# Performance work log

Measured on AMD Instinct MI355X. Metric: run time of the kernel, lower is better.

## Reference

```python
import jax, jax.numpy as jnp
import numpy as np

L = 4; B = 128; S = 128; N = B * S; E = 262144
IN = 64; HID = 128; PE = 16; HEADS = 4; DK = HID // HEADS; OUT = 10


def setup_inputs() -> dict:
    key = jax.random.key(0)
    ks = iter(jax.random.split(key, 64))
    def nrm(shape, scale=1.0):
        return jax.random.normal(next(ks), shape, jnp.float32) * scale
    inp = {
        'x': nrm((N, IN)),
        'pe': nrm((N, PE)),
        'edge_attr': nrm((E, HID)),
        'sph': jax.random.uniform(next(ks), (B, 1, S, S), jnp.float32),
        'node_w': nrm((IN, HID - PE), 0.05), 'node_b': jnp.zeros((HID - PE,), jnp.float32),
        'pe_w': nrm((PE, PE), 0.05), 'pe_b': jnp.zeros((PE,), jnp.float32),
        'conv_Aw': nrm((L, HID, HID), 0.05), 'conv_Ab': jnp.zeros((L, HID), jnp.float32),
        'conv_Bw': nrm((L, HID, HID), 0.05), 'conv_Bb': jnp.zeros((L, HID), jnp.float32),
        'conv_Cw': nrm((L, HID, HID), 0.05), 'conv_Cb': jnp.zeros((L, HID), jnp.float32),
        'conv_Dw': nrm((L, HID, HID), 0.05), 'conv_Db': jnp.zeros((L, HID), jnp.float32),
        'conv_Ew': nrm((L, HID, HID), 0.05), 'conv_Eb': jnp.zeros((L, HID), jnp.float32),
        'bnx_g': jnp.ones((L, HID), jnp.float32), 'bnx_b': jnp.zeros((L, HID), jnp.float32),
        'bne_g': jnp.ones((L, HID), jnp.float32), 'bne_b': jnp.zeros((L, HID), jnp.float32),
        'attn_w': nrm((4, HID, HID), 0.05), 'attn_b': jnp.zeros((4, HID), jnp.float32),
        'mlp1_w': nrm((HID, HID // 2), 0.05), 'mlp1_b': jnp.zeros((HID // 2,), jnp.float32),
        'mlp2_w': nrm((HID // 2, HID // 4), 0.05), 'mlp2_b': jnp.zeros((HID // 4,), jnp.float32),
        'mlp3_w': nrm((HID // 4, OUT), 0.05), 'mlp3_b': jnp.zeros((OUT,), jnp.float32),
        'edge_index': jax.random.randint(next(ks), (2, E), 0, N, dtype=jnp.int32),
        'batch': jnp.repeat(jnp.arange(B, dtype=jnp.int32), S),  # equal-size graphs, sorted
    }
    return inp


def _bn(v, g, b):
    # BatchNorm1d in training mode (batch statistics), eps=1e-5
    mu = v.mean(0)
    var = jnp.mean((v - mu) ** 2, 0)
    return g * (v - mu) * jax.lax.rsqrt(var + 1e-5) + b


def _forward(x, pe, edge_attr, sph, node_w, node_b, pe_w, pe_b,
             conv_Aw, conv_Ab, conv_Bw, conv_Bb, conv_Cw, conv_Cb,
             conv_Dw, conv_Db, conv_Ew, conv_Eb,
             bnx_g, bnx_b, bne_g, bne_b, attn_w, attn_b,
             mlp1_w, mlp1_b, mlp2_w, mlp2_b, mlp3_w, mlp3_b,
             edge_index, batch):
    src, dst = edge_index[0], edge_index[1]  # message j->i: index = dst
    h = jnp.concatenate([x @ node_w + node_b, pe @ pe_w + pe_b], axis=-1)  # [N, HID]
    e = edge_attr
    inv_sqrt_dk = np.float32(1.0 / np.sqrt(DK))
    for l in range(L):
        # ---- GatedGCNConv (residual, aggr='add' with sigmoid-gated normalization) ----
        Ax = h @ conv_Aw[l] + conv_Ab[l]
        Bx = h @ conv_Bw[l] + conv_Bb[l]
        Ce = e @ conv_Cw[l] + conv_Cb[l]
        Dx = h @ conv_Dw[l] + conv_Db[l]
        Ex = h @ conv_Ew[l] + conv_Eb[l]
        e_ij = Dx[dst] + Ex[src] + Ce               # [E, HID] pre-sigmoid edge feature
        sigma = jax.nn.sigmoid(e_ij)
        num = jax.ops.segment_sum(sigma * Bx[src], dst, num_segments=N)
        den = jax.ops.segment_sum(sigma, dst, num_segments=N)
        h_new = Ax + num / (den + 1e-6)
        h = jax.nn.relu(_bn(h_new, bnx_g[l], bnx_b[l])) + h
        e = jax.nn.relu(_bn(e_ij, bne_g[l], bne_b[l])) + e
        # ---- dense MHA with sph score bias (to_dense_batch == reshape, equal-size graphs) ----
        xd = h.reshape(B, S, HID)
        q = (xd @ attn_w[0] + attn_b[0]).reshape(B, S, HEADS, DK).transpose(0, 2, 1, 3)
        k = (xd @ attn_w[1] + attn_b[1]).reshape(B, S, HEADS, DK).transpose(0, 2, 1, 3)
        v = (xd @ attn_w[2] + attn_b[2]).reshape(B, S, HEADS, DK).transpose(0, 2, 1, 3)
        scores = jnp.einsum('bhsd,bhtd->bhst', q, k) * inv_sqrt_dk
        p = jax.nn.softmax(scores * sph, axis=-1)
        o = jnp.einsum('bhst,bhtd->bhsd', p, v).transpose(0, 2, 1, 3).reshape(B, S, HID)
        h = (o @ attn_w[3] + attn_b[3]).reshape(N, HID)
    # global mean pool over each graph
    g = jax.ops.segment_sum(h, batch, num_segments=B) / np.float32(S)
    g = jax.nn.relu(g @ mlp1_w + mlp1_b)
    g = jax.nn.relu(g @ mlp2_w + mlp2_b)
    return g @ mlp3_w + mlp3_b  # [B, OUT]


def reference(x, pe, edge_attr, sph, node_w, node_b, pe_w, pe_b,
              conv_Aw, conv_Ab, conv_Bw, conv_Bb, conv_Cw, conv_Cb,
              conv_Dw, conv_Db, conv_Ew, conv_Eb,
              bnx_g, bnx_b, bne_g, bne_b, attn_w, attn_b,
              mlp1_w, mlp1_b, mlp2_w, mlp2_b, mlp3_w, mlp3_b,
              edge_index, batch):
    return _forward(x, pe, edge_attr, sph, node_w, node_b, pe_w, pe_b,
                    conv_Aw, conv_Ab, conv_Bw, conv_Bb, conv_Cw, conv_Cb,
                    conv_Dw, conv_Db, conv_Ew, conv_Eb,
                    bnx_g, bnx_b, bne_g, bne_b, attn_w, attn_b,
                    mlp1_w, mlp1_b, mlp2_w, mlp2_b, mlp3_w, mlp3_b,
                    edge_index, batch)
```

## Files before the change

### kernel.cpp

```cpp
#include <hip/hip_runtime.h>
#include <math.h>

#define L_LAYERS 4
#define B_G 128
#define S_G 128
#define N_N 16384
#define E_E 262144
#define IN_F 64
#define HID 128
#define PE_F 16
#define HEADS 4
#define DK 32
#define OUT_F 10

typedef __bf16 bf16x8 __attribute__((ext_vector_type(8)));
typedef float f32x4 __attribute__((ext_vector_type(4)));

struct Sel4 { float* o[4]; const float* b[4]; int slot[4]; };
struct WSrc24 { const float* w[24]; };

__global__ void zero_int_kernel(int* __restrict__ p, int n) {
    int i = blockIdx.x * 256 + threadIdx.x;
    if (i < n) p[i] = 0;
}

__global__ void hist_kernel(const int* __restrict__ dst, int* __restrict__ deg) {
    int e = blockIdx.x * 256 + threadIdx.x;
    if (e < E_E) atomicAdd(&deg[dst[e]], 1);
}

__global__ __launch_bounds__(1024) void scan_kernel(const int* __restrict__ deg,
                                                    int* __restrict__ row_ptr,
                                                    int* __restrict__ cursor) {
    __shared__ int lds[1024];
    int tid = threadIdx.x;
    int base = tid * 16;
    int d[16];
    int s = 0;
#pragma unroll
    for (int i = 0; i < 16; i++) { d[i] = deg[base + i]; s += d[i]; }
    lds[tid] = s;
    __syncthreads();
    for (int off = 1; off < 1024; off <<= 1) {
        int v = (tid >= off) ? lds[tid - off] : 0;
        __syncthreads();
        lds[tid] += v;
        __syncthreads();
    }
    int run = lds[tid] - s;
#pragma unroll
    for (int i = 0; i < 16; i++) {
        row_ptr[base + i] = run;
        cursor[base + i] = run;
        run += d[i];
    }
    if (tid == 1023) row_ptr[N_N] = run;
}

__global__ void scatter_kernel(const int* __restrict__ src, const int* __restrict__ dst,
                               int* __restrict__ cursor, int* __restrict__ perm,
                               int* __restrict__ ssrc, int* __restrict__ sdst) {
    int e = blockIdx.x * 256 + threadIdx.x;
    if (e >= E_E) return;
    int dd = dst[e];
    int pos = atomicAdd(&cursor[dd], 1);
    perm[pos] = e;
    ssrc[pos] = src[e];
    sdst[pos] = dd;
}

__global__ __launch_bounds__(256) void pack_w_kernel(WSrc24 ws, __bf16* __restrict__ Whi,
                                                     __bf16* __restrict__ Wlo) {
    int m = blockIdx.x >> 2, part = blockIdx.x & 3;
    const float* W = ws.w[m];
    int tid = threadIdx.x;
    for (int i = part * 16; i < part * 16 + 16; i++) {
        int p = i * 256 + tid;
        int j = p & 7, lane = (p >> 3) & 63, kc = (p >> 9) & 3, nt = p >> 11;
        int k = kc * 32 + (lane >> 4) * 8 + j;
        int n = nt * 16 + (lane & 15);
        float w = W[k * 128 + n];
        __bf16 h = (__bf16)w;
        Whi[(long)m * 16384 + p] = h;
        Wlo[(long)m * 16384 + p] = (__bf16)(w - (float)h);
    }
}

__global__ void embed_kernel(const float* __restrict__ x, const float* __restrict__ pe,
                             const float* __restrict__ node_w, const float* __restrict__ node_b,
                             const float* __restrict__ pe_w, const float* __restrict__ pe_b,
                             float* __restrict__ h) {
    int idx = blockIdx.x * 256 + threadIdx.x;
    if (idx >= N_N * HID) return;
    int i = idx >> 7, c = idx & 127;
    float acc;
    if (c < 112) {
        acc = node_b[c];
        const float* xr = x + (long)i * IN_F;
        for (int k = 0; k < IN_F; k++) acc += xr[k] * node_w[k * 112 + c];
    } else {
        int cc = c - 112;
        acc = pe_b[cc];
        const float* pr = pe + (long)i * PE_F;
        for (int k = 0; k < PE_F; k++) acc += pr[k] * pe_w[k * PE_F + cc];
    }
    h[idx] = acc;
}

template <int MODE>
__global__ __launch_bounds__(256) void mfma_gemm_kernel(
    const float* __restrict__ A, const int* __restrict__ perm,
    const __bf16* __restrict__ Whi, const __bf16* __restrict__ Wlo, Sel4 sel,
    const float* __restrict__ Dx, const float* __restrict__ Ex,
    const int* __restrict__ sdst, const int* __restrict__ ssrc,
    float* __restrict__ stats_acc) {
    __shared__ float sred[1024];
    int tid = threadIdx.x;
    int lane = tid & 63, wave = tid >> 6;
    int l15 = lane & 15, quad = lane >> 4;
    int y = blockIdx.y;
    float* out = sel.o[y];
    const float* bias = sel.b[y];
    const bf16x8* whv = (const bf16x8*)(Whi + (long)sel.slot[y] * 16384);
    const bf16x8* wlv = (const bf16x8*)(Wlo + (long)sel.slot[y] * 16384);

    long r0 = (long)blockIdx.x * 128 + wave * 32;
    long ra0 = r0 + l15, ra1 = r0 + 16 + l15;
    if (MODE == 1 && perm) { ra0 = perm[ra0]; ra1 = perm[ra1]; }

    float4 av[2][8];
    {
        const float* Ap0 = A + ra0 * 128 + quad * 8;
        const float* Ap1 = A + ra1 * 128 + quad * 8;
#pragma unroll
        for (int kc = 0; kc < 4; kc++) {
            av[0][kc * 2] = *(const float4*)(Ap0 + kc * 32);
            av[0][kc * 2 + 1] = *(const float4*)(Ap0 + kc * 32 + 4);
            av[1][kc * 2] = *(const float4*)(Ap1 + kc * 32);
            av[1][kc * 2 + 1] = *(const float4*)(Ap1 + kc * 32 + 4);
        }
    }
    bf16x8 ahi[2][4], alo[2][4];
#pragma unroll
    for (int t = 0; t < 2; t++)
#pragma unroll
        for (int kc = 0; kc < 4; kc++) {
            float fv[8] = {av[t][kc * 2].x, av[t][kc * 2].y, av[t][kc * 2].z, av[t][kc * 2].w,
                           av[t][kc * 2 + 1].x, av[t][kc * 2 + 1].y, av[t][kc * 2 + 1].z,
                           av[t][kc * 2 + 1].w};
#pragma unroll
            for (int j = 0; j < 8; j++) {
                __bf16 hh = (__bf16)fv[j];
                ahi[t][kc][j] = hh;
                alo[t][kc][j] = (__bf16)(fv[j] - (float)hh);
            }
        }

    f32x4 acc[2][8];
#pragma unroll
    for (int t = 0; t < 2; t++)
#pragma unroll
        for (int nt = 0; nt < 8; nt++) acc[t][nt] = (f32x4){0.f, 0.f, 0.f, 0.f};

#pragma unroll
    for (int nt = 0; nt < 8; nt++) {
#pragma unroll
        for (int kc = 0; kc < 4; kc++) {
            bf16x8 bhi = whv[(nt * 4 + kc) * 64 + lane];
            bf16x8 blo = wlv[(nt * 4 + kc) * 64 + lane];
            acc[0][nt] = __builtin_amdgcn_mfma_f32_16x16x32_bf16(ahi[0][kc], blo, acc[0][nt], 0, 0, 0);
            acc[1][nt] = __builtin_amdgcn_mfma_f32_16x16x32_bf16(ahi[1][kc], blo, acc[1][nt], 0, 0, 0);
            acc[0][nt] = __builtin_amdgcn_mfma_f32_16x16x32_bf16(alo[0][kc], bhi, acc[0][nt], 0, 0, 0);
            acc[1][nt] = __builtin_amdgcn_mfma_f32_16x16x32_bf16(alo[1][kc], bhi, acc[1][nt], 0, 0, 0);
            acc[0][nt] = __builtin_amdgcn_mfma_f32_16x16x32_bf16(ahi[0][kc], bhi, acc[0][nt], 0, 0, 0);
            acc[1][nt] = __builtin_amdgcn_mfma_f32_16x16x32_bf16(ahi[1][kc], bhi, acc[1][nt], 0, 0, 0);
        }
    }

    float csum[8], csq[8];
#pragma unroll
    for (int nt = 0; nt < 8; nt++) { csum[nt] = 0.f; csq[nt] = 0.f; }

#pragma unroll
    for (int t = 0; t < 2; t++) {
        long rb = r0 + t * 16 + quad * 4;
        int sd[4], ss[4];
        if (MODE == 1) {
#pragma unroll
            for (int r = 0; r < 4; r++) { sd[r] = sdst[rb + r]; ss[r] = ssrc[rb + r]; }
        }
#pragma unroll
        for (int nt = 0; nt < 8; nt++) {
            int c = nt * 16 + l15;
            float bb = bias[c];
#pragma unroll
            for (int r = 0; r < 4; r++) {
                float v = acc[t][nt][r] + bb;
                if (MODE == 1) v += Dx[(long)sd[r] * 128 + c] + Ex[(long)ss[r] * 128 + c];
                out[(rb + r) * 128 + c] = v;
                if (MODE == 1) { csum[nt] += v; csq[nt] += v * v; }
            }
        }
    }

    if (MODE == 1) {
#pragma unroll
        for (int nt = 0; nt < 8; nt++) {
            float s = csum[nt];
            s += __shfl_xor(s, 16); s += __shfl_xor(s, 32);
            float q = csq[nt];
            q += __shfl_xor(q, 16); q += __shfl_xor(q, 32);
            if (quad == 0) {
                sred[wave * 256 + nt * 16 + l15] = s;
                sred[wave * 256 + 128 + nt * 16 + l15] = q;
            }
        }
        __syncthreads();
        if (tid < 256) {
            float v = sred[tid] + sred[256 + tid] + sred[512 + tid] + sred[768 + tid];
            atomicAdd(&stats_acc[tid], v);
        }
    }
}

__global__ void ebn_finalize_kernel(const float* __restrict__ acc, float invM,
                                    float* __restrict__ stat) {
    int c = threadIdx.x;
    float mu = acc[c] * invM;
    float var = acc[128 + c] * invM - mu * mu;
    stat[c] = mu;
    stat[128 + c] = rsqrtf(var + 1e-5f);
}

__global__ __launch_bounds__(256) void bn_stats_kernel(const float* __restrict__ v, long M,
                                                       float* __restrict__ partial) {
    __shared__ float lds[256];
    int tid = threadIdx.x;
    int c = tid & 127, half = tid >> 7;
    float sum = 0.f, sq = 0.f;
    for (long r = (long)blockIdx.x * 2 + half; r < M; r += (long)gridDim.x * 2) {
        float x = v[r * 128 + c];
        sum += x; sq += x * x;
    }
    lds[tid] = sum;
    __syncthreads();
    if (half == 0) sum += lds[tid + 128];
    __syncthreads();
    lds[tid] = sq;
    __syncthreads();
    if (half == 0) {
        sq += lds[tid + 128];
        partial[(long)blockIdx.x * 256 + c] = sum;
        partial[(long)blockIdx.x * 256 + 128 + c] = sq;
    }
}

__global__ void bn_finalize_kernel(const float* __restrict__ partial, int nblk, float invM,
                                   float* __restrict__ stat) {
    int c = threadIdx.x;
    float s = 0.f, q = 0.f;
    for (int i = 0; i < nblk; i++) {
        s += partial[i * 256 + c];
        q += partial[i * 256 + 128 + c];
    }
    float mu = s * invM;
    float var = q * invM - mu * mu;
    stat[c] = mu;
    stat[128 + c] = rsqrtf(var + 1e-5f);
}

__global__ void bn_apply_res_kernel(const float* __restrict__ vin, const float* __restrict__ stat,
                                    const float* __restrict__ g, const float* __restrict__ b,
                                    float* __restrict__ io, long M4) {
    long idx = (long)blockIdx.x * 256 + threadIdx.x;
    if (idx >= M4) return;
    int c4 = (idx & 31) << 2;
    float4 x = ((const float4*)vin)[idx];
    float4 res = ((float4*)io)[idx];
    float xv[4] = {x.x, x.y, x.z, x.w};
    float rv[4] = {res.x, res.y, res.z, res.w};
    float o[4];
#pragma unroll
    for (int t = 0; t < 4; t++) {
        int c = c4 + t;
        float y = g[c] * (xv[t] - stat[c]) * stat[128 + c] + b[c];
        o[t] = fmaxf(y, 0.f) + rv[t];
    }
    ((float4*)io)[idx] = make_float4(o[0], o[1], o[2], o[3]);
}

__global__ __launch_bounds__(256) void agg_bn_kernel(
    const float* __restrict__ eij, const float* __restrict__ Bx, const float* __restrict__ Ax,
    const int* __restrict__ row_ptr, const int* __restrict__ ssrc,
    const float* __restrict__ estat, const float* __restrict__ g, const float* __restrict__ b,
    const float* __restrict__ eold, const int* __restrict__ perm,
    float* __restrict__ e_out, float* __restrict__ hnew) {
    int wave = threadIdx.x >> 6, lane = threadIdx.x & 63;
    int i = blockIdx.x * 4 + wave;
    int c = lane << 1;
    int s0 = row_ptr[i], s1 = row_ptr[i + 1];
    float2 mu = *(const float2*)&estat[c];
    float2 rs = *(const float2*)&estat[128 + c];
    float2 gg = *(const float2*)&g[c];
    float2 bb = *(const float2*)&b[c];
    float nx = 0.f, ny = 0.f, dx = 0.f, dy = 0.f;

    int j = s0;
    for (; j + 2 <= s1; j += 2) {
        int src0 = ssrc[j], src1 = ssrc[j + 1];
        long er0 = perm ? (long)perm[j] : (long)j;
        long er1 = perm ? (long)perm[j + 1] : (long)(j + 1);
        float2 x0 = *(const float2*)&eij[(long)j * 128 + c];
        float2 x1 = *(const float2*)&eij[(long)(j + 1) * 128 + c];
        float2 bx0 = *(const float2*)&Bx[(long)src0 * 128 + c];
        float2 bx1 = *(const float2*)&Bx[(long)src1 * 128 + c];
        float2 o0 = *(const float2*)&eold[er0 * 128 + c];
        float2 o1 = *(const float2*)&eold[er1 * 128 + c];
        float s0x = 1.f / (1.f + __expf(-x0.x)), s0y = 1.f / (1.f + __expf(-x0.y));
        float s1x = 1.f / (1.f + __expf(-x1.x)), s1y = 1.f / (1.f + __expf(-x1.y));
        nx += s0x * bx0.x + s1x * bx1.x;
        ny += s0y * bx0.y + s1y * bx1.y;
        dx += s0x + s1x;
        dy += s0y + s1y;
        float2 y0, y1;
        y0.x = fmaxf(gg.x * (x0.x - mu.x) * rs.x + bb.x, 0.f) + o0.x;
        y0.y = fmaxf(gg.y * (x0.y - mu.y) * rs.y + bb.y, 0.f) + o0.y;
        y1.x = fmaxf(gg.x * (x1.x - mu.x) * rs.x + bb.x, 0.f) + o1.x;
        y1.y = fmaxf(gg.y * (x1.y - mu.y) * rs.y + bb.y, 0.f) + o1.y;
        *(float2*)&e_out[(long)j * 128 + c] = y0;
        *(float2*)&e_out[(long)(j + 1) * 128 + c] = y1;
    }
    if (j < s1) {
        int src0 = ssrc[j];
        long er0 = perm ? (long)perm[j] : (long)j;
        float2 x0 = *(const float2*)&eij[(long)j * 128 + c];
        float2 bx0 = *(const float2*)&Bx[(long)src0 * 128 + c];
        float2 o0 = *(const float2*)&eold[er0 * 128 + c];
        float s0x = 1.f / (1.f + __expf(-x0.x)), s0y = 1.f / (1.f + __expf(-x0.y));
        nx += s0x * bx0.x; ny += s0y * bx0.y;
        dx += s0x; dy += s0y;
        float2 y0;
        y0.x = fmaxf(gg.x * (x0.x - mu.x) * rs.x + bb.x, 0.f) + o0.x;
        y0.y = fmaxf(gg.y * (x0.y - mu.y) * rs.y + bb.y, 0.f) + o0.y;
        *(float2*)&e_out[(long)j * 128 + c] = y0;
    }

    long idx = (long)i * 128 + c;
    float2 ax = *(const float2*)&Ax[idx];
    float2 hv;
    hv.x = ax.x + nx / (dx + 1e-6f);
    hv.y = ax.y + ny / (dy + 1e-6f);
    *(float2*)&hnew[idx] = hv;
}

__global__ __launch_bounds__(256) void attn_kernel(const float* __restrict__ q,
                                                   const float* __restrict__ k,
                                                   const float* __restrict__ v,
                                                   const float* __restrict__ sph,
                                                   float* __restrict__ o) {
    __shared__ float k_lds[128 * 32];
    __shared__ float v_lds[128 * 32];
    int b = blockIdx.x >> 2, hd = blockIdx.x & 3;
    int tid = threadIdx.x;

    for (int i = tid; i < 1024; i += 256) {
        int t = i >> 3, d4 = i & 7;
        long gidx = (long)(b * 128 + t) * 32 + hd * 8 + d4;
        ((float4*)k_lds)[t * 8 + d4] = ((const float4*)k)[gidx];
        ((float4*)v_lds)[t * 8 + d4] = ((const float4*)v)[gidx];
    }
    __syncthreads();

    int s = tid >> 1, t0 = (tid & 1) * 64;
    float4 qreg[8];
    long qbase = (long)(b * 128 + s) * 32 + hd * 8;
#pragma unroll
    for (int j = 0; j < 8; j++) qreg[j] = ((const float4*)q)[qbase + j];
    const float* sphrow = sph + ((long)b * 128 + s) * 128 + t0;
    const float inv_sqrt_dk = 0.17677669529663687f;

    float p[64];
#pragma unroll
    for (int i = 0; i < 64; i++) {
        const float4* kr = (const float4*)&k_lds[(t0 + i) * 32];
        float acc = 0.f;
#pragma unroll
        for (int j = 0; j < 8; j++) {
            float4 kv = kr[j];
            acc += qreg[j].x * kv.x + qreg[j].y * kv.y + qreg[j].z * kv.z + qreg[j].w * kv.w;
        }
        p[i] = acc * inv_sqrt_dk * sphrow[i];
    }
    float m = -1e30f;
#pragma unroll
    for (int i = 0; i < 64; i++) m = fmaxf(m, p[i]);
    m = fmaxf(m, __shfl_xor(m, 1));
    float l = 0.f;
#pragma unroll
    for (int i = 0; i < 64; i++) {
        p[i] = __expf(p[i] - m);
        l += p[i];
    }
    l += __shfl_xor(l, 1);
    float invl = 1.f / l;

    float part[32];
#pragma unroll
    for (int d = 0; d < 32; d++) part[d] = 0.f;
#pragma unroll
    for (int i = 0; i < 64; i++) {
        float pv = p[i] * invl;
        const float4* vr = (const float4*)&v_lds[(t0 + i) * 32];
#pragma unroll
        for (int j = 0; j < 8; j++) {
            float4 vv = vr[j];
            part[4 * j + 0] += pv * vv.x;
            part[4 * j + 1] += pv * vv.y;
            part[4 * j + 2] += pv * vv.z;
            part[4 * j + 3] += pv * vv.w;
        }
    }
    int halfw = tid & 1;
    float outv[16];
#pragma unroll
    for (int d = 0; d < 32; d++) {
        float tot = part[d] + __shfl_xor(part[d], 1);
        if ((d >> 4) == halfw) outv[d & 15] = tot;
    }
    long obase = (long)(b * 128 + s) * 32 + hd * 8 + halfw * 4;
#pragma unroll
    for (int j = 0; j < 4; j++)
        ((float4*)o)[obase + j] = make_float4(outv[4 * j], outv[4 * j + 1], outv[4 * j + 2], outv[4 * j + 3]);
}

__global__ __launch_bounds__(128) void pool_mlp_kernel(
    const float* __restrict__ h, const float* __restrict__ w1, const float* __restrict__ b1,
    const float* __restrict__ w2, const float* __restrict__ b2, const float* __restrict__ w3,
    const float* __restrict__ b3, float* __restrict__ out) {
    __shared__ float g[128], m1[64], m2[32];
    int b = blockIdx.x, tid = threadIdx.x;
    const float* hb = h + (long)b * 128 * 128;
    float s = 0.f;
    for (int r = 0; r < 128; r++) s += hb[r * 128 + tid];
    g[tid] = s * (1.f / 128.f);
    __syncthreads();
    if (tid < 64) {
        float a = b1[tid];
        for (int kk = 0; kk < 128; kk++) a += g[kk] * w1[kk * 64 + tid];
        m1[tid] = fmaxf(a, 0.f);
    }
    __syncthreads();
    if (tid < 32) {
        float a = b2[tid];
        for (int kk = 0; kk < 64; kk++) a += m1[kk] * w2[kk * 32 + tid];
        m2[tid] = fmaxf(a, 0.f);
    }
    __syncthreads();
    if (tid < 10) {
        float a = b3[tid];
        for (int kk = 0; kk < 32; kk++) a += m2[kk] * w3[kk * 10 + tid];
        out[b * 10 + tid] = a;
    }
}

extern "C" void kernel_launch(void* const* d_in, const int* in_sizes, int n_in,
                              void* d_out, int out_size, void* d_ws, size_t ws_size,
                              hipStream_t stream) {
    (void)in_sizes; (void)n_in; (void)out_size;
    const float* x        = (const float*)d_in[0];
    const float* pe       = (const float*)d_in[1];
    const float* edge_attr= (const float*)d_in[2];
    const float* sph      = (const float*)d_in[3];
    const float* node_w   = (const float*)d_in[4];
    const float* node_b   = (const float*)d_in[5];
    const float* pe_w     = (const float*)d_in[6];
    const float* pe_b     = (const float*)d_in[7];
    const float* conv_Aw  = (const float*)d_in[8];
    const float* conv_Ab  = (const float*)d_in[9];
    const float* conv_Bw  = (const float*)d_in[10];
    const float* conv_Bb  = (const float*)d_in[11];
    const float* conv_Cw  = (const float*)d_in[12];
    const float* conv_Cb  = (const float*)d_in[13];
    const float* conv_Dw  = (const float*)d_in[14];
    const float* conv_Db  = (const float*)d_in[15];
    const float* conv_Ew  = (const float*)d_in[16];
    const float* conv_Eb  = (const float*)d_in[17];
    const float* bnx_g    = (const float*)d_in[18];
    const float* bnx_b    = (const float*)d_in[19];
    const float* bne_g    = (const float*)d_in[20];
    const float* bne_b    = (const float*)d_in[21];
    const float* attn_w   = (const float*)d_in[22];
    const float* attn_b   = (const float*)d_in[23];
    const float* mlp1_w   = (const float*)d_in[24];
    const float* mlp1_b   = (const float*)d_in[25];
    const float* mlp2_w   = (const float*)d_in[26];
    const float* mlp2_b   = (const float*)d_in[27];
    const float* mlp3_w   = (const float*)d_in[28];
    const float* mlp3_b   = (const float*)d_in[29];
    const int*   eidx     = (const int*)d_in[30];
    const int* esrc = eidx;
    const int* edst = eidx + E_E;
    float* out = (float*)d_out;

    float* f = (float*)d_ws;
    float* h      = f; f += (long)N_N * HID;
    float* hnew   = f; f += (long)N_N * HID;
    float* Ax     = f; f += (long)N_N * HID;
    float* Bx     = f; f += (long)N_N * HID;
    float* Dx     = f; f += (long)N_N * HID;
    float* Ex     = f; f += (long)N_N * HID;
    float* e      = f; f += (long)E_E * HID;
    float* eij    = f; f += (long)E_E * HID;
    float* partial= f; f += 512 * 256;
    float* bnxs   = f; f += 256;
    float* bnes   = f; f += 256;
    float* ebn_acc= f; f += 256;
    __bf16* Whi = (__bf16*)f;
    __bf16* Wlo = Whi + 24 * 16384;
    int* ip = (int*)(Wlo + 24 * 16384);
    int* deg     = ip; ip += N_N;
    int* row_ptr = ip; ip += N_N + 1;
    int* cursor  = ip; ip += N_N;
    int* perm    = ip; ip += E_E;
    int* ssrc    = ip; ip += E_E;
    int* sdst    = ip; ip += E_E;
    size_t need = (size_t)((char*)ip - (char*)d_ws);
    if (ws_size < need) return;

    WSrc24 wsrc;
    for (int l = 0; l < L_LAYERS; l++) {
        wsrc.w[l * 5 + 0] = conv_Aw + l * 16384;
        wsrc.w[l * 5 + 1] = conv_Bw + l * 16384;
        wsrc.w[l * 5 + 2] = conv_Cw + l * 16384;
        wsrc.w[l * 5 + 3] = conv_Dw + l * 16384;
        wsrc.w[l * 5 + 4] = conv_Ew + l * 16384;
    }
    for (int m = 0; m < 4; m++) wsrc.w[20 + m] = attn_w + m * 16384;
    pack_w_kernel<<<96, 256, 0, stream>>>(wsrc, Whi, Wlo);

    zero_int_kernel<<<(N_N + 255) / 256, 256, 0, stream>>>(deg, N_N);
    hist_kernel<<<E_E / 256, 256, 0, stream>>>(edst, deg);
    scan_kernel<<<1, 1024, 0, stream>>>(deg, row_ptr, cursor);
    scatter_kernel<<<E_E / 256, 256, 0, stream>>>(esrc, edst, cursor, perm, ssrc, sdst);

    embed_kernel<<<N_N * HID / 256, 256, 0, stream>>>(x, pe, node_w, node_b, pe_w, pe_b, h);

    for (int l = 0; l < L_LAYERS; l++) {
        zero_int_kernel<<<1, 256, 0, stream>>>((int*)ebn_acc, 256);

        Sel4 selN;
        selN.o[0] = Ax; selN.b[0] = conv_Ab + l * 128; selN.slot[0] = l * 5 + 0;
        selN.o[1] = Bx; selN.b[1] = conv_Bb + l * 128; selN.slot[1] = l * 5 + 1;
        selN.o[2] = Dx; selN.b[2] = conv_Db + l * 128; selN.slot[2] = l * 5 + 3;
        selN.o[3] = Ex; selN.b[3] = conv_Eb + l * 128; selN.slot[3] = l * 5 + 4;
        mfma_gemm_kernel<0><<<dim3(N_N / 128, 4), 256, 0, stream>>>(
            h, nullptr, Whi, Wlo, selN, nullptr, nullptr, nullptr, nullptr, nullptr);

        const float* Asrc = (l == 0) ? edge_attr : e;
        const int* permA = (l == 0) ? perm : nullptr;
        Sel4 selE;
        selE.o[0] = eij; selE.b[0] = conv_Cb + l * 128; selE.slot[0] = l * 5 + 2;
        selE.o[1] = selE.o[2] = selE.o[3] = eij;
        selE.b[1] = selE.b[2] = selE.b[3] = selE.b[0];
        selE.slot[1] = selE.slot[2] = selE.slot[3] = selE.slot[0];
        mfma_gemm_kernel<1><<<dim3(E_E / 128, 1), 256, 0, stream>>>(
            Asrc, permA, Whi, Wlo, selE, Dx, Ex, sdst, ssrc, ebn_acc);

        ebn_finalize_kernel<<<1, 128, 0, stream>>>(ebn_acc, 1.f / E_E, bnes);

        const float* eoldSrc = (l == 0) ? edge_attr : e;
        const int* permE = (l == 0) ? perm : nullptr;
        agg_bn_kernel<<<N_N / 4, 256, 0, stream>>>(eij, Bx, Ax, row_ptr, ssrc, bnes,
                                                   bne_g + l * 128, bne_b + l * 128,
                                                   eoldSrc, permE, e, hnew);

        bn_stats_kernel<<<128, 256, 0, stream>>>(hnew, (long)N_N, partial);
        bn_finalize_kernel<<<1, 128, 0, stream>>>(partial, 128, 1.f / N_N, bnxs);
        bn_apply_res_kernel<<<N_N * 32 / 256, 256, 0, stream>>>(
            hnew, bnxs, bnx_g + l * 128, bnx_b + l * 128, h, (long)N_N * 32);

        Sel4 selQ;
        selQ.o[0] = Ax; selQ.b[0] = attn_b;       selQ.slot[0] = 20;
        selQ.o[1] = Bx; selQ.b[1] = attn_b + 128; selQ.slot[1] = 21;
        selQ.o[2] = Dx; selQ.b[2] = attn_b + 256; selQ.slot[2] = 22;
        selQ.o[3] = Dx; selQ.b[3] = attn_b + 256; selQ.slot[3] = 22;
        mfma_gemm_kernel<0><<<dim3(N_N / 128, 3), 256, 0, stream>>>(
            h, nullptr, Whi, Wlo, selQ, nullptr, nullptr, nullptr, nullptr, nullptr);

        attn_kernel<<<B_G * HEADS, 256, 0, stream>>>(Ax, Bx, Dx, sph, Ex);

        Sel4 selP;
        selP.o[0] = h; selP.b[0] = attn_b + 384; selP.slot[0] = 23;
        selP.o[1] = selP.o[2] = selP.o[3] = h;
        selP.b[1] = selP.b[2] = selP.b[3] = selP.b[0];
        selP.slot[1] = selP.slot[2] = selP.slot[3] = selP.slot[0];
        mfma_gemm_kernel<0><<<dim3(N_N / 128, 1), 256, 0, stream>>>(
            Ex, nullptr, Whi, Wlo, selP, nullptr, nullptr, nullptr, nullptr, nullptr);
    }

    pool_mlp_kernel<<<B_G, 128, 0, stream>>>(h, mlp1_w, mlp1_b, mlp2_w, mlp2_b, mlp3_w, mlp3_b, out);
}
```

Baseline: 2.050 ms.

## Shrink GEMM tile to 16 rows per wave and replicate BN stat accumulators

Each wave in the MFMA GEMM now handles one 16-row tile instead of two, and A-operand loads are streamed per K-chunk instead of held in registers up front. This cuts register pressure so more waves fit, and the grid doubles. Weight fragments are now reloaded for every 16 rows instead of every 32, which doubles weight traffic. The edge-BN statistics atomics are also spread over 32 replicated accumulators to reduce atomic contention, with the finalize kernel summing the replicas.

```diff
diff --git a/kernel.cpp b/kernel.cpp
--- a/kernel.cpp
+++ b/kernel.cpp
@@ -18,6 +18,8 @@
 
 struct Sel4 { float* o[4]; const float* b[4]; int slot[4]; };
 struct WSrc24 { const float* w[24]; };
+
+#define STATS_REP 32
 
 __global__ void zero_int_kernel(int* __restrict__ p, int n) {
     int i = blockIdx.x * 256 + threadIdx.x;
@@ -118,88 +120,67 @@
     int tid = threadIdx.x;
     int lane = tid & 63, wave = tid >> 6;
     int l15 = lane & 15, quad = lane >> 4;
+    long rowBase = (long)blockIdx.x * 64 + wave * 16;
     int y = blockIdx.y;
     float* out = sel.o[y];
     const float* bias = sel.b[y];
     const bf16x8* whv = (const bf16x8*)(Whi + (long)sel.slot[y] * 16384);
     const bf16x8* wlv = (const bf16x8*)(Wlo + (long)sel.slot[y] * 16384);
 
-    long r0 = (long)blockIdx.x * 128 + wave * 32;
-    long ra0 = r0 + l15, ra1 = r0 + 16 + l15;
-    if (MODE == 1 && perm) { ra0 = perm[ra0]; ra1 = perm[ra1]; }
-
-    float4 av[2][8];
-    {
-        const float* Ap0 = A + ra0 * 128 + quad * 8;
-        const float* Ap1 = A + ra1 * 128 + quad * 8;
-#pragma unroll
-        for (int kc = 0; kc < 4; kc++) {
-            av[0][kc * 2] = *(const float4*)(Ap0 + kc * 32);
-            av[0][kc * 2 + 1] = *(const float4*)(Ap0 + kc * 32 + 4);
-            av[1][kc * 2] = *(const float4*)(Ap1 + kc * 32);
-            av[1][kc * 2 + 1] = *(const float4*)(Ap1 + kc * 32 + 4);
-        }
-    }
-    bf16x8 ahi[2][4], alo[2][4];
-#pragma unroll
-    for (int t = 0; t < 2; t++)
-#pragma unroll
-        for (int kc = 0; kc < 4; kc++) {
-            float fv[8] = {av[t][kc * 2].x, av[t][kc * 2].y, av[t][kc * 2].z, av[t][kc * 2].w,
-                           av[t][kc * 2 + 1].x, av[t][kc * 2 + 1].y, av[t][kc * 2 + 1].z,
-                           av[t][kc * 2 + 1].w};
-#pragma unroll
-            for (int j = 0; j < 8; j++) {
-                __bf16 hh = (__bf16)fv[j];
-                ahi[t][kc][j] = hh;
-                alo[t][kc][j] = (__bf16)(fv[j] - (float)hh);
-            }
-        }
-
-    f32x4 acc[2][8];
-#pragma unroll
-    for (int t = 0; t < 2; t++)
-#pragma unroll
-        for (int nt = 0; nt < 8; nt++) acc[t][nt] = (f32x4){0.f, 0.f, 0.f, 0.f};
-
-#pragma unroll
-    for (int nt = 0; nt < 8; nt++) {
-#pragma unroll
-        for (int kc = 0; kc < 4; kc++) {
+    long arow = rowBase + l15;
+    if (MODE == 1 && perm) arow = perm[arow];
+    const float* Ap = A + arow * 128 + quad * 8;
+
+    f32x4 acc[8];
+#pragma unroll
+    for (int t = 0; t < 8; t++) acc[t] = (f32x4){0.f, 0.f, 0.f, 0.f};
+
+#pragma unroll
+    for (int kc = 0; kc < 4; kc++) {
+        float4 a0 = *(const float4*)(Ap + kc * 32);
+        float4 a1 = *(const float4*)(Ap + kc * 32 + 4);
+        float f[8] = {a0.x, a0.y, a0.z, a0.w, a1.x, a1.y, a1.z, a1.w};
+        bf16x8 ahi, alo;
+#pragma unroll
+        for (int j = 0; j < 8; j++) {
+            __bf16 hh = (__bf16)f[j];
+            ahi[j] = hh;
+            alo[j] = (__bf16)(f[j] - (float)hh);
+        }
+#pragma unroll
+        for (int nt = 0; nt < 8; nt++) {
             bf16x8 bhi = whv[(nt * 4 + kc) * 64 + lane];
             bf16x8 blo = wlv[(nt * 4 + kc) * 64 + lane];
-            acc[0][nt] = __builtin_amdgcn_mfma_f32_16x16x32_bf16(ahi[0][kc], blo, acc[0][nt], 0, 0, 0);
-            acc[1][nt] = __builtin_amdgcn_mfma_f32_16x16x32_bf16(ahi[1][kc], blo, acc[1][nt], 0, 0, 0);
-            acc[0][nt] = __builtin_amdgcn_mfma_f32_16x16x32_bf16(alo[0][kc], bhi, acc[0][nt], 0, 0, 0);
-            acc[1][nt] = __builtin_amdgcn_mfma_f32_16x16x32_bf16(alo[1][kc], bhi, acc[1][nt], 0, 0, 0);
-            acc[0][nt] = __builtin_amdgcn_mfma_f32_16x16x32_bf16(ahi[0][kc], bhi, acc[0][nt], 0, 0, 0);
-            acc[1][nt] = __builtin_amdgcn_mfma_f32_16x16x32_bf16(ahi[1][kc], bhi, acc[1][nt], 0, 0, 0);
-        }
-    }
-
+            acc[nt] = __builtin_amdgcn_mfma_f32_16x16x32_bf16(ahi, blo, acc[nt], 0, 0, 0);
+            acc[nt] = __builtin_amdgcn_mfma_f32_16x16x32_bf16(alo, bhi, acc[nt], 0, 0, 0);
+            acc[nt] = __builtin_amdgcn_mfma_f32_16x16x32_bf16(ahi, bhi, acc[nt], 0, 0, 0);
+        }
+    }
+
+    int sd[4], ss[4];
+    if (MODE == 1) {
+#pragma unroll
+        for (int r = 0; r < 4; r++) {
+            long row = rowBase + quad * 4 + r;
+            sd[r] = sdst[row];
+            ss[r] = ssrc[row];
+        }
+    }
     float csum[8], csq[8];
 #pragma unroll
     for (int nt = 0; nt < 8; nt++) { csum[nt] = 0.f; csq[nt] = 0.f; }
 
 #pragma unroll
-    for (int t = 0; t < 2; t++) {
-        long rb = r0 + t * 16 + quad * 4;
-        int sd[4], ss[4];
-        if (MODE == 1) {
-#pragma unroll
-            for (int r = 0; r < 4; r++) { sd[r] = sdst[rb + r]; ss[r] = ssrc[rb + r]; }
-        }
-#pragma unroll
-        for (int nt = 0; nt < 8; nt++) {
-            int c = nt * 16 + l15;
-            float bb = bias[c];
-#pragma unroll
-            for (int r = 0; r < 4; r++) {
-                float v = acc[t][nt][r] + bb;
-                if (MODE == 1) v += Dx[(long)sd[r] * 128 + c] + Ex[(long)ss[r] * 128 + c];
-                out[(rb + r) * 128 + c] = v;
-                if (MODE == 1) { csum[nt] += v; csq[nt] += v * v; }
-            }
+    for (int nt = 0; nt < 8; nt++) {
+        int c = nt * 16 + l15;
+        float bb = bias[c];
+#pragma unroll
+        for (int r = 0; r < 4; r++) {
+            long row = rowBase + quad * 4 + r;
+            float v = acc[nt][r] + bb;
+            if (MODE == 1) v += Dx[(long)sd[r] * 128 + c] + Ex[(long)ss[r] * 128 + c];
+            out[row * 128 + c] = v;
+            if (MODE == 1) { csum[nt] += v; csq[nt] += v * v; }
         }
     }
 
@@ -218,7 +199,7 @@
         __syncthreads();
         if (tid < 256) {
             float v = sred[tid] + sred[256 + tid] + sred[512 + tid] + sred[768 + tid];
-            atomicAdd(&stats_acc[tid], v);
+            atomicAdd(&stats_acc[(blockIdx.x & (STATS_REP - 1)) * 256 + tid], v);
         }
     }
 }
@@ -226,8 +207,13 @@
 __global__ void ebn_finalize_kernel(const float* __restrict__ acc, float invM,
                                     float* __restrict__ stat) {
     int c = threadIdx.x;
-    float mu = acc[c] * invM;
-    float var = acc[128 + c] * invM - mu * mu;
+    float s = 0.f, q = 0.f;
+    for (int r = 0; r < STATS_REP; r++) {
+        s += acc[r * 256 + c];
+        q += acc[r * 256 + 128 + c];
+    }
+    float mu = s * invM;
+    float var = q * invM - mu * mu;
     stat[c] = mu;
     stat[128 + c] = rsqrtf(var + 1e-5f);
 }
@@ -514,7 +500,7 @@
     float* partial= f; f += 512 * 256;
     float* bnxs   = f; f += 256;
     float* bnes   = f; f += 256;
-    float* ebn_acc= f; f += 256;
+    float* ebn_acc= f; f += STATS_REP * 256;
     __bf16* Whi = (__bf16*)f;
     __bf16* Wlo = Whi + 24 * 16384;
     int* ip = (int*)(Wlo + 24 * 16384);
@@ -546,14 +532,14 @@
     embed_kernel<<<N_N * HID / 256, 256, 0, stream>>>(x, pe, node_w, node_b, pe_w, pe_b, h);
 
     for (int l = 0; l < L_LAYERS; l++) {
-        zero_int_kernel<<<1, 256, 0, stream>>>((int*)ebn_acc, 256);
+        zero_int_kernel<<<STATS_REP, 256, 0, stream>>>((int*)ebn_acc, STATS_REP * 256);
 
         Sel4 selN;
         selN.o[0] = Ax; selN.b[0] = conv_Ab + l * 128; selN.slot[0] = l * 5 + 0;
         selN.o[1] = Bx; selN.b[1] = conv_Bb + l * 128; selN.slot[1] = l * 5 + 1;
         selN.o[2] = Dx; selN.b[2] = conv_Db + l * 128; selN.slot[2] = l * 5 + 3;
         selN.o[3] = Ex; selN.b[3] = conv_Eb + l * 128; selN.slot[3] = l * 5 + 4;
-        mfma_gemm_kernel<0><<<dim3(N_N / 128, 4), 256, 0, stream>>>(
+        mfma_gemm_kernel<0><<<dim3(N_N / 64, 4), 256, 0, stream>>>(
             h, nullptr, Whi, Wlo, selN, nullptr, nullptr, nullptr, nullptr, nullptr);
 
         const float* Asrc = (l == 0) ? edge_attr : e;
@@ -563,7 +549,7 @@
         selE.o[1] = selE.o[2] = selE.o[3] = eij;
         selE.b[1] = selE.b[2] = selE.b[3] = selE.b[0];
         selE.slot[1] = selE.slot[2] = selE.slot[3] = selE.slot[0];
-        mfma_gemm_kernel<1><<<dim3(E_E / 128, 1), 256, 0, stream>>>(
+        mfma_gemm_kernel<1><<<dim3(E_E / 64, 1), 256, 0, stream>>>(
             Asrc, permA, Whi, Wlo, selE, Dx, Ex, sdst, ssrc, ebn_acc);
 
         ebn_finalize_kernel<<<1, 128, 0, stream>>>(ebn_acc, 1.f / E_E, bnes);
@@ -584,7 +570,7 @@
         selQ.o[1] = Bx; selQ.b[1] = attn_b + 128; selQ.slot[1] = 21;
         selQ.o[2] = Dx; selQ.b[2] = attn_b + 256; selQ.slot[2] = 22;
         selQ.o[3] = Dx; selQ.b[3] = attn_b + 256; selQ.slot[3] = 22;
-        mfma_gemm_kernel<0><<<dim3(N_N / 128, 3), 256, 0, stream>>>(
+        mfma_gemm_kernel<0><<<dim3(N_N / 64, 3), 256, 0, stream>>>(
             h, nullptr, Whi, Wlo, selQ, nullptr, nullptr, nullptr, nullptr, nullptr);
 
         attn_kernel<<<B_G * HEADS, 256, 0, stream>>>(Ax, Bx, Dx, sph, Ex);
@@ -594,7 +580,7 @@
         selP.o[1] = selP.o[2] = selP.o[3] = h;
         selP.b[1] = selP.b[2] = selP.b[3] = selP.b[0];
         selP.slot[1] = selP.slot[2] = selP.slot[3] = selP.slot[0];
-        mfma_gemm_kernel<0><<<dim3(N_N / 128, 1), 256, 0, stream>>>(
+        mfma_gemm_kernel<0><<<dim3(N_N / 64, 1), 256, 0, stream>>>(
             Ex, nullptr, Whi, Wlo, selP, nullptr, nullptr, nullptr, nullptr, nullptr);
     }
 
```

New measurement: 1.785 ms. 12.9% less time.
